# Kernel optimization log

Hardware: AMD Instinct MI355X
Metric: run time of the kernel (lower is better)

Reference implementation:

```python
import jax, jax.numpy as jnp
import numpy as np
from jax import lax

FEAT_STRIDE = 16
SCALES = (8, 16, 32)
RATIOS = (0.5, 1.0, 2.0)
PRE_NMS = 6000
POST_NMS = 300
NMS_THRESH = 0.7
MIN_SIZE = 16.0


def _base_anchors():
    base = 16.0
    cx = cy = base / 2.0
    anchors = []
    for r in RATIOS:
        for s in SCALES:
            h = base * s * np.sqrt(r)
            w = base * s * np.sqrt(1.0 / r)
            anchors.append([cx - w / 2, cy - h / 2, cx + w / 2, cy + h / 2])
    return np.asarray(anchors, np.float32)  # [A,4] (x1,y1,x2,y2)


def _shifted_anchors(h, w):
    base = _base_anchors()
    sy = np.arange(h, dtype=np.float32) * FEAT_STRIDE
    sx = np.arange(w, dtype=np.float32) * FEAT_STRIDE
    yy, xx = np.meshgrid(sy, sx, indexing='ij')  # h-major then w, matching NHWC permute
    shifts = np.stack([xx, yy, xx, yy], axis=-1).reshape(-1, 1, 4)
    return (shifts + base[None]).reshape(-1, 4).astype(np.float32)  # [h*w*A,4]


def _conv(x, w, b, pad):
    y = lax.conv_general_dilated(x, w, (1, 1), [(pad, pad), (pad, pad)],
                                 dimension_numbers=('NCHW', 'OIHW', 'NCHW'))
    return y + b[None, :, None, None]


def _iou(box, boxes):
    lt = jnp.maximum(box[:2], boxes[:, :2])
    rb = jnp.minimum(box[2:], boxes[:, 2:])
    wh = jnp.maximum(rb - lt, 0.0)
    inter = wh[:, 0] * wh[:, 1]
    a1 = (box[2] - box[0]) * (box[3] - box[1])
    a2 = (boxes[:, 2] - boxes[:, 0]) * (boxes[:, 3] - boxes[:, 1])
    return inter / (a1 + a2 - inter + 1e-9)


def _nms_proposals(boxes, scores):
    # boxes [K,4], scores [K] -> [POST_NMS,4]
    ws = boxes[:, 2] - boxes[:, 0]
    hs = boxes[:, 3] - boxes[:, 1]
    scores = jnp.where((ws >= MIN_SIZE) & (hs >= MIN_SIZE), scores, -jnp.inf)
    top_s, idx = lax.top_k(scores, PRE_NMS)
    b = boxes[idx]

    def body(i, st):
        keep, s = st
        j = jnp.argmax(s).astype(jnp.int32)
        keep = keep.at[i].set(j)
        sup = _iou(b[j], b) >= NMS_THRESH  # suppresses j itself too (iou=1)
        s = jnp.where(sup, -jnp.inf, s)
        return keep, s

    keep, _ = lax.fori_loop(0, POST_NMS, body,
                            (jnp.zeros((POST_NMS,), jnp.int32), top_s))
    return b[keep]


def setup_inputs() -> dict:
    key = jax.random.key(0)
    ks = jax.random.split(key, 5)
    n, c, h, w = 8, 512, 50, 64
    A = len(SCALES) * len(RATIOS)
    x = jax.random.normal(ks[0], (n, c, h, w), jnp.float32)
    w1 = jax.random.normal(ks[1], (512, 512, 3, 3), jnp.float32) * 0.02
    b1 = jnp.zeros((512,), jnp.float32)
    w_cls = jax.random.normal(ks[2], (A * 2, 512, 1, 1), jnp.float32) * 0.02
    b_cls = jnp.zeros((A * 2,), jnp.float32)
    w_bbox = jax.random.normal(ks[3], (A * 4, 512, 1, 1), jnp.float32) * 0.005
    b_bbox = jnp.zeros((A * 4,), jnp.float32)
    return {'x': x, 'w1': w1, 'b1': b1, 'w_cls': w_cls, 'b_cls': b_cls,
            'w_bbox': w_bbox, 'b_bbox': b_bbox}


def reference(x, w1, b1, w_cls, b_cls, w_bbox, b_bbox):
    n, _, h, w = x.shape
    A = len(SCALES) * len(RATIOS)
    img_h, img_w = h * FEAT_STRIDE, w * FEAT_STRIDE
    anchors = jnp.asarray(_shifted_anchors(h, w))  # [h*w*A,4]

    feat = jax.nn.relu(_conv(x, w1, b1, 1))
    cls = _conv(feat, w_cls, b_cls, 0).transpose(0, 2, 3, 1).reshape(n, h, w, A, 2)
    fg = jax.nn.softmax(cls, axis=-1)[..., 1].reshape(n, -1)  # [n, h*w*A]
    deltas = _conv(feat, w_bbox, b_bbox, 0).transpose(0, 2, 3, 1).reshape(n, -1, 4)

    # decode deltas against anchors
    aw = anchors[:, 2] - anchors[:, 0]
    ah = anchors[:, 3] - anchors[:, 1]
    acx = anchors[:, 0] + 0.5 * aw
    acy = anchors[:, 1] + 0.5 * ah
    cx = deltas[..., 0] * aw + acx
    cy = deltas[..., 1] * ah + acy
    pw = jnp.exp(deltas[..., 2]) * aw
    ph = jnp.exp(deltas[..., 3]) * ah
    boxes = jnp.stack([cx - 0.5 * pw, cy - 0.5 * ph,
                       cx + 0.5 * pw, cy + 0.5 * ph], axis=-1)  # [n,K,4]
    hi = jnp.asarray([img_w, img_h, img_w, img_h], jnp.float32)
    boxes = jnp.clip(boxes, 0.0, hi)

    rois = jax.vmap(_nms_proposals)(boxes, fg)  # [n,POST_NMS,4]
    roi_indices = jnp.repeat(jnp.arange(n, dtype=jnp.int32), POST_NMS)
    return rois.reshape(-1, 4), roi_indices
```

## Files before the change

### kernel.cpp

```cpp
#include <hip/hip_runtime.h>
#include <math.h>

#define NIMG 8
#define CIN  512
#define HF   50
#define WF   64
#define HW   3200
#define NA   9
#define KPER 28800
#define PRE  6000
#define POST 300

#define WHT_ELEMS  32768

#define NW    94
#define NCAP  6016

#define XTROWS 52
#define XTCOLS 66
#define XT_ELEMS ((size_t)NIMG * XTROWS * XTCOLS * CIN)
#define XT_BYTES (XT_ELEMS * 2)

#define WPK_ELEMS ((size_t)2 * 4 * 9 * 16 * 4096)
#define WPK_HALF  (4 * 9 * 16 * 4096)

#define SCALE_X 256.0f
#define SCALE_W 16384.0f
#define INV_SCALE (1.0f / 4194304.0f)

typedef _Float16 f16x8 __attribute__((ext_vector_type(8)));
typedef float f32x4  __attribute__((ext_vector_type(4)));
typedef unsigned short u16x8 __attribute__((ext_vector_type(8)));
typedef unsigned long long u64;

__constant__ float BASEA[9][4] = {
  {-82.509667991878083f, -37.254833995939042f,  98.509667991878083f,  53.254833995939042f},
  {-173.01933598375617f, -82.509667991878083f, 189.01933598375617f,   98.509667991878083f},
  {-354.03867196751233f, -173.01933598375617f, 370.03867196751233f,  189.01933598375617f},
  { -56.0f,  -56.0f,  72.0f,  72.0f},
  {-120.0f, -120.0f, 136.0f, 136.0f},
  {-248.0f, -248.0f, 264.0f, 264.0f},
  {-37.254833995939042f, -82.509667991878083f,  53.254833995939042f,  98.509667991878083f},
  {-82.509667991878083f, -173.01933598375617f,  98.509667991878083f, 189.01933598375617f},
  {-173.01933598375617f, -354.03867196751233f, 189.01933598375617f,  370.03867196751233f},
};

__device__ __forceinline__ unsigned int ordf(float f) {
  unsigned int u = __float_as_uint(f);
  return (u & 0x80000000u) ? ~u : (u | 0x80000000u);
}

__device__ __forceinline__ unsigned short f2h(float f) {
  union { _Float16 h; unsigned short u; } cv;
  cv.h = (_Float16)f;
  return cv.u;
}
__device__ __forceinline__ float h2f(unsigned short u) {
  union { _Float16 h; unsigned short u; } cv;
  cv.u = u;
  return (float)cv.h;
}

__global__ __launch_bounds__(256) void k_zerox(float4* __restrict__ a,
                                               float4* __restrict__ b) {
  const int tot = (int)(XT_BYTES / 16);
  const int stride = gridDim.x * 256;
  const float4 z = make_float4(0.f, 0.f, 0.f, 0.f);
  for (int i = blockIdx.x * 256 + threadIdx.x; i < tot; i += stride) {
    a[i] = z;
    b[i] = z;
  }
}

__global__ __launch_bounds__(256) void k_prepxT(const float4* __restrict__ x4,
                                                unsigned short* __restrict__ xh,
                                                unsigned short* __restrict__ xl) {
  __shared__ float tile[128][65];
  const int b = blockIdx.x;
  const int cic = b & 3;
  const int rest = b >> 2;
  const int hrow = rest % 50;
  const int n = rest / 50;
  const int t = threadIdx.x;
#pragma unroll
  for (int jj = 0; jj < 8; ++jj) {
    const int e = t + 256 * jj;
    const int row = e >> 4, c4 = e & 15;
    const float4 v = x4[(((size_t)(n * CIN + cic * 128 + row) * HF + hrow) << 4) + c4];
    tile[row][c4 * 4 + 0] = v.x;
    tile[row][c4 * 4 + 1] = v.y;
    tile[row][c4 * 4 + 2] = v.z;
    tile[row][c4 * 4 + 3] = v.w;
  }
  __syncthreads();
#pragma unroll
  for (int jj = 0; jj < 4; ++jj) {
    const int e = t + 256 * jj;
    const int w = e >> 4, c8 = e & 15;
    const size_t base = ((size_t)((n * XTROWS + (hrow + 1)) * XTCOLS) + (w + 1)) * CIN
                        + cic * 128 + c8 * 8;
    u16x8 hv, lv;
#pragma unroll
    for (int u = 0; u < 8; ++u) {
      const float g = tile[c8 * 8 + u][w] * SCALE_X;
      const unsigned short hh = f2h(g);
      hv[u] = (short)hh;
      lv[u] = (short)f2h(g - h2f(hh));
    }
    *reinterpret_cast<u16x8*>(xh + base) = hv;
    *reinterpret_cast<u16x8*>(xl + base) = lv;
  }
}

__global__ __launch_bounds__(256) void k_prepwPk(const float* __restrict__ w1,
                                                 unsigned short* __restrict__ wpk) {
  const int tot = (int)WPK_ELEMS;
  const int stride = gridDim.x * 256;
  for (int idx = blockIdx.x * 256 + threadIdx.x; idx < tot; idx += stride) {
    const int i = idx & 4095;
    int rest = idx >> 12;
    const int ks = rest & 15; rest >>= 4;
    const int tap = rest % 9; rest /= 9;
    const int cob = rest & 3;
    const int sp = rest >> 2;
    const int col = i >> 5;
    const int slotp = (i >> 3) & 3;
    const int j = i & 7;
    const int s = slotp ^ ((col >> 1) & 3);
    const int ci = ks * 32 + s * 8 + j;
    const int co = cob * 128 + col;
    const float g = w1[((size_t)co * CIN + ci) * 9 + tap] * SCALE_W;
    const unsigned short hh = f2h(g);
    wpk[idx] = sp ? f2h(g - h2f(hh)) : hh;
  }
}

__global__ __launch_bounds__(256) void k_preph(const float* __restrict__ wc,
                                               const float* __restrict__ bc,
                                               const float* __restrict__ wb,
                                               const float* __restrict__ bb,
                                               float* __restrict__ WHT2,
                                               float* __restrict__ bh) {
  const int TOT = WHT_ELEMS + 64;
  const int stride = gridDim.x * 256;
  for (int idx = blockIdx.x * 256 + threadIdx.x; idx < TOT; idx += stride) {
    if (idx < WHT_ELEMS) {
      int r = idx & 3;
      int o = (idx >> 2) & 63;
      int c = (idx >> 8) * 4 + r;
      float v = 0.0f;
      if (o < 18) v = wc[(size_t)o * CIN + c];
      else if (o < 54) v = wb[(size_t)(o - 18) * CIN + c];
      WHT2[idx] = v;
    } else {
      int o = idx - WHT_ELEMS;
      float v = 0.0f;
      if (o < 18) v = bc[o];
      else if (o < 54) v = bb[o - 18];
      bh[o] = v;
    }
  }
}

#define GLDS(gp, lp) __builtin_amdgcn_global_load_lds( \
    (const __attribute__((address_space(1))) unsigned int*)(gp), \
    (__attribute__((address_space(3))) unsigned int*)(lp), 16, 0, 0)

__global__ __launch_bounds__(256, 2) void k_convmfma(
    const unsigned short* __restrict__ xh,
    const unsigned short* __restrict__ xl,
    const unsigned short* __restrict__ wpk,
    const float* __restrict__ b1,
    float* __restrict__ feat) {
  __shared__ unsigned short lds[2][4][4096];

  const int pb  = blockIdx.x;
  const int cob = blockIdx.y;
  const int n   = pb / 25;
  const int h0  = (pb - n * 25) * 2;
  const int t   = threadIdx.x;
  const int wid = t >> 6;
  const int l   = t & 63;
  const int wm  = wid >> 1;
  const int wn  = wid & 1;

  const int colp = l >> 2;
  const int sB = (((l & 3) ^ ((l >> 3) & 3)) << 3);
  const unsigned short* xsrc = (wid == 3) ? xl : xh;
  const size_t wA_base = (size_t)(wid & 1) * WPK_HALF;

  const int fr = l & 15;
  const int fq = l >> 4;
  const int slotr = ((fq ^ ((fr >> 1) & 3)) << 4);

  f32x4 acc[4][4] = {};

  auto stage = [&](int sbuf, int ti) {
    const int ks  = ti / 9;
    const int tap = ti - ks * 9;
    if (wid < 2) {
      const unsigned short* gp = wpk + wA_base
          + ((size_t)((cob * 9 + tap) * 16 + ks) << 12) + l * 8;
      unsigned short* lp = &lds[sbuf][wid][0];
#pragma unroll
      for (int q = 0; q < 8; ++q)
        GLDS(gp + q * 512, lp + q * 512);
    } else {
      const int ky = (tap * 11) >> 5;
      const int kx = tap - ky * 3;
      const size_t ebase = ((size_t)((n * XTROWS + h0 + ky) * XTCOLS + kx + colp) << 9)
                           + ks * 32 + sB;
      unsigned short* lp = &lds[sbuf][wid][0];
#pragma unroll
      for (int q = 0; q < 8; ++q)
        GLDS(xsrc + ebase + ((size_t)(((q >> 2) * XTCOLS + (q & 3) * 16)) << 9),
             lp + q * 512);
    }
  };

  stage(0, 0);
  __syncthreads();

  int buf = 0;
  for (int ti = 0; ti < 144; ++ti) {
    if (ti < 143) stage(buf ^ 1, ti + 1);

    f16x8 ah[4], al[4], bhf[4], blf[4];
#pragma unroll
    for (int mi = 0; mi < 4; ++mi) {
      const int off = (((wm << 6) + (mi << 4) + fr) << 6) + slotr;
      ah[mi] = *(const f16x8*)((const char*)&lds[buf][0][0] + off);
      al[mi] = *(const f16x8*)((const char*)&lds[buf][1][0] + off);
    }
#pragma unroll
    for (int ni = 0; ni < 4; ++ni) {
      const int off = (((wn << 6) + (ni << 4) + fr) << 6) + slotr;
      bhf[ni] = *(const f16x8*)((const char*)&lds[buf][2][0] + off);
      blf[ni] = *(const f16x8*)((const char*)&lds[buf][3][0] + off);
    }
#pragma unroll
    for (int mi = 0; mi < 4; ++mi)
#pragma unroll
      for (int ni = 0; ni < 4; ++ni) {
        acc[mi][ni] = __builtin_amdgcn_mfma_f32_16x16x32_f16(ah[mi], bhf[ni], acc[mi][ni], 0, 0, 0);
        acc[mi][ni] = __builtin_amdgcn_mfma_f32_16x16x32_f16(ah[mi], blf[ni], acc[mi][ni], 0, 0, 0);
        acc[mi][ni] = __builtin_amdgcn_mfma_f32_16x16x32_f16(al[mi], bhf[ni], acc[mi][ni], 0, 0, 0);
      }
    __syncthreads();
    buf ^= 1;
  }

  const int h = h0 + wn;
#pragma unroll
  for (int mi = 0; mi < 4; ++mi) {
    const int co = (cob << 7) + (wm << 6) + (mi << 4) + (fq << 2);
    const float4 bias = *(const float4*)&b1[co];
#pragma unroll
    for (int ni = 0; ni < 4; ++ni) {
      const int w = (ni << 4) + fr;
      float4 v;
      v.x = fmaxf(fmaf(acc[mi][ni][0], INV_SCALE, bias.x), 0.0f);
      v.y = fmaxf(fmaf(acc[mi][ni][1], INV_SCALE, bias.y), 0.0f);
      v.z = fmaxf(fmaf(acc[mi][ni][2], INV_SCALE, bias.z), 0.0f);
      v.w = fmaxf(fmaf(acc[mi][ni][3], INV_SCALE, bias.w), 0.0f);
      *(float4*)(feat + (((size_t)n * HW + h * WF + w) << 9) + co) = v;
    }
  }
}

__global__ __launch_bounds__(256) void k_head(const float* __restrict__ feat,
                                              const float* __restrict__ WHT2,
                                              const float* __restrict__ bh,
                                              float* __restrict__ scores,
                                              float4* __restrict__ boxes) {
  __shared__ float fsh[16][512];
  __shared__ float vsh[16][64];
  const int t = threadIdx.x;
  const int wvid = t >> 6;
  const int o = t & 63;
  const int pos0 = blockIdx.x * 16;

  for (int i = t; i < 16 * 512; i += 256)
    fsh[i >> 9][i & 511] = feat[((size_t)pos0 << 9) + i];
  __syncthreads();

  {
    const int p0 = wvid * 4;
    float a0 = 0.f, a1 = 0.f, a2 = 0.f, a3 = 0.f;
    const float4* wp = reinterpret_cast<const float4*>(WHT2);
    const float4* f0 = reinterpret_cast<const float4*>(&fsh[p0 + 0][0]);
    const float4* f1 = reinterpret_cast<const float4*>(&fsh[p0 + 1][0]);
    const float4* f2 = reinterpret_cast<const float4*>(&fsh[p0 + 2][0]);
    const float4* f3 = reinterpret_cast<const float4*>(&fsh[p0 + 3][0]);
#pragma unroll 4
    for (int c4 = 0; c4 < 128; ++c4) {
      float4 w4 = wp[c4 * 64 + o];
      float4 v;
      v = f0[c4];
      a0 = fmaf(w4.x, v.x, a0); a0 = fmaf(w4.y, v.y, a0);
      a0 = fmaf(w4.z, v.z, a0); a0 = fmaf(w4.w, v.w, a0);
      v = f1[c4];
      a1 = fmaf(w4.x, v.x, a1); a1 = fmaf(w4.y, v.y, a1);
      a1 = fmaf(w4.z, v.z, a1); a1 = fmaf(w4.w, v.w, a1);
      v = f2[c4];
      a2 = fmaf(w4.x, v.x, a2); a2 = fmaf(w4.y, v.y, a2);
      a2 = fmaf(w4.z, v.z, a2); a2 = fmaf(w4.w, v.w, a2);
      v = f3[c4];
      a3 = fmaf(w4.x, v.x, a3); a3 = fmaf(w4.y, v.y, a3);
      a3 = fmaf(w4.z, v.z, a3); a3 = fmaf(w4.w, v.w, a3);
    }
    float bv = bh[o];
    vsh[p0 + 0][o] = a0 + bv;
    vsh[p0 + 1][o] = a1 + bv;
    vsh[p0 + 2][o] = a2 + bv;
    vsh[p0 + 3][o] = a3 + bv;
  }
  __syncthreads();

  if (t < 144) {
    const int p2 = t / 9, a = t % 9;
    const int pos = pos0 + p2;
    const int n = pos / HW;
    const int r = pos - n * HW;
    const int ph = r >> 6;
    const int pw = r & 63;

    float l0 = vsh[p2][a * 2];
    float l1 = vsh[p2][a * 2 + 1];
    float m  = fmaxf(l0, l1);
    float e0 = (float)exp((double)__fsub_rn(l0, m));
    float e1 = (float)exp((double)__fsub_rn(l1, m));
    float fg = __fdiv_rn(e1, __fadd_rn(e0, e1));

    float d0 = vsh[p2][18 + a * 4 + 0];
    float d1 = vsh[p2][18 + a * 4 + 1];
    float d2 = vsh[p2][18 + a * 4 + 2];
    float d3 = vsh[p2][18 + a * 4 + 3];

    float sx = (float)(pw * 16);
    float sy = (float)(ph * 16);
    float ax1 = __fadd_rn(BASEA[a][0], sx);
    float ay1 = __fadd_rn(BASEA[a][1], sy);
    float ax2 = __fadd_rn(BASEA[a][2], sx);
    float ay2 = __fadd_rn(BASEA[a][3], sy);
    float aw = __fsub_rn(ax2, ax1);
    float ah = __fsub_rn(ay2, ay1);
    float acx = __fadd_rn(ax1, __fmul_rn(0.5f, aw));
    float acy = __fadd_rn(ay1, __fmul_rn(0.5f, ah));
    float cx = __fadd_rn(__fmul_rn(d0, aw), acx);
    float cy = __fadd_rn(__fmul_rn(d1, ah), acy);
    float pwd = __fmul_rn((float)exp((double)d2), aw);
    float phd = __fmul_rn((float)exp((double)d3), ah);
    float x1 = __fsub_rn(cx, __fmul_rn(0.5f, pwd));
    float y1 = __fsub_rn(cy, __fmul_rn(0.5f, phd));
    float x2 = __fadd_rn(cx, __fmul_rn(0.5f, pwd));
    float y2 = __fadd_rn(cy, __fmul_rn(0.5f, phd));
    x1 = fminf(fmaxf(x1, 0.0f), 1024.0f);
    x2 = fminf(fmaxf(x2, 0.0f), 1024.0f);
    y1 = fminf(fmaxf(y1, 0.0f), 800.0f);
    y2 = fminf(fmaxf(y2, 0.0f), 800.0f);
    float wsz = __fsub_rn(x2, x1);
    float hsz = __fsub_rn(y2, y1);
    float sc = (wsz >= 16.0f && hsz >= 16.0f) ? fg : -__builtin_huge_valf();

    const int idx = n * KPER + r * NA + a;
    scores[idx] = sc;
    boxes[idx] = make_float4(x1, y1, x2, y2);
  }
}

__global__ __launch_bounds__(1024) void k_topk(const float* __restrict__ scores,
                                               u64* __restrict__ ckey) {
  const int n = blockIdx.x;
  const int t = threadIdx.x;
  __shared__ unsigned int hist[256];
  __shared__ unsigned int sh_selB, sh_ngt, sh_binc, sh_num;
  const float* sc = scores + (size_t)n * KPER;

  unsigned int prefix = 0, prefMask = 0, ngt = 0, neq = 0;
  for (int shift = 24; shift >= 0; shift -= 8) {
    if (t < 256) hist[t] = 0;
    __syncthreads();
    for (int i = t; i < KPER; i += 1024) {
      unsigned int u = ordf(sc[i]);
      if ((u & prefMask) == prefix) atomicAdd(&hist[(u >> shift) & 255], 1u);
    }
    __syncthreads();
    if (t == 0) {
      unsigned int cnt = ngt;
      for (int b = 255; b >= 0; --b) {
        unsigned int c = hist[b];
        if (cnt + c >= (unsigned)PRE) { sh_selB = (unsigned)b; sh_ngt = cnt; sh_binc = c; break; }
        cnt += c;
      }
    }
    __syncthreads();
    prefix |= (sh_selB << shift);
    prefMask |= (0xFFu << shift);
    ngt = sh_ngt;
    neq = sh_binc;
    __syncthreads();
  }
  const unsigned int T = prefix;
  const unsigned int needed = (unsigned)PRE - ngt;
  unsigned int J = 0xFFFFFFFFu;
  if (needed < neq) {
    if (t < 256) hist[t] = 0;
    __syncthreads();
    for (int i = t; i < KPER; i += 1024)
      if (ordf(sc[i]) == T) atomicAdd(&hist[i >> 7], 1u);
    __syncthreads();
    if (t == 0) {
      unsigned int cnt = 0;
      for (int b = 0; b < 256; ++b) {
        unsigned int c = hist[b];
        if (cnt + c >= needed) { sh_selB = (unsigned)b; sh_ngt = needed - cnt; break; }
        cnt += c;
      }
    }
    __syncthreads();
    const unsigned int selH = sh_selB;
    const unsigned int needLow = sh_ngt;
    __syncthreads();
    if (t < 128) hist[t] = 0;
    __syncthreads();
    for (int i = t; i < KPER; i += 1024)
      if (ordf(sc[i]) == T && ((unsigned)(i >> 7)) == selH) atomicAdd(&hist[i & 127], 1u);
    __syncthreads();
    if (t == 0) {
      unsigned int cnt = 0;
      for (int b = 0; b < 128; ++b) {
        unsigned int c = hist[b];
        if (cnt + c >= needLow) { sh_selB = (selH << 7) | (unsigned)b; break; }
        cnt += c;
      }
    }
    __syncthreads();
    J = sh_selB;
  }

  if (t == 0) sh_num = 0;
  __syncthreads();
  for (int i = t; i < KPER; i += 1024) {
    unsigned int u = ordf(sc[i]);
    bool in = (u > T) || (u == T && (unsigned)i <= J);
    if (in) {
      unsigned int p = atomicAdd(&sh_num, 1u);
      ckey[(size_t)n * PRE + p] = (((u64)u) << 32) | (u64)(~(unsigned int)i);
    }
  }
}

__global__ __launch_bounds__(1024) void k_sortc(const u64* __restrict__ ckey,
                                                const float4* __restrict__ boxes,
                                                float4* __restrict__ sbox,
                                                u64* __restrict__ valid) {
  __shared__ u64 sk[8192];
  const int n = blockIdx.x;
  const int t = threadIdx.x;
  for (int e = t; e < 8192; e += 1024)
    sk[e] = (e < PRE) ? ckey[(size_t)n * PRE + e] : 0ull;
  __syncthreads();
  for (int k = 2; k <= 8192; k <<= 1) {
    for (int j = k >> 1; j > 0; j >>= 1) {
      for (int p = t; p < 4096; p += 1024) {
        const int i = ((p & ~(j - 1)) << 1) | (p & (j - 1));
        const int ip = i | j;
        u64 a = sk[i], b = sk[ip];
        const bool desc = ((i & k) == 0);
        if ((a < b) == desc) { sk[i] = b; sk[ip] = a; }
      }
      __syncthreads();
    }
  }
  for (int e = t; e < NCAP; e += 1024) {
    float4 bx = make_float4(0.f, 0.f, 0.f, 0.f);
    if (e < PRE) {
      unsigned idx = ~(unsigned)(sk[e] & 0xFFFFFFFFull);
      bx = boxes[(size_t)n * KPER + idx];
    }
    sbox[(size_t)n * NCAP + e] = bx;
  }
  if (t < 128) {
    u64 w = 0;
    if (t < NW) {
      for (int b = 0; b < 64; ++b) {
        int e = t * 64 + b;
        if (e < PRE && ((sk[e] >> 32) > 0x007FFFFFull)) w |= 1ull << b;
      }
    }
    valid[n * 128 + t] = w;
  }
}

__global__ __launch_bounds__(64) void k_mask(const float4* __restrict__ sbox,
                                             u64* __restrict__ mask) {
  const int ib = blockIdx.x;
  const int jb = blockIdx.y;
  const int n  = blockIdx.z;
  const int r  = threadIdx.x;
  const int i  = ib * 64 + r;
  u64* mout = mask + ((size_t)(n * NCAP) + i) * NW + jb;
  if (jb < ib) { *mout = 0ull; return; }
  __shared__ float4 jbox[64];
  jbox[r] = sbox[(size_t)n * NCAP + jb * 64 + r];
  __syncthreads();
  const float4 p = sbox[(size_t)n * NCAP + i];
  const float pa = __fmul_rn(__fsub_rn(p.z, p.x), __fsub_rn(p.w, p.y));
  u64 word = 0;
#pragma unroll 8
  for (int b = 0; b < 64; ++b) {
    const float4 q = jbox[b];
    float ltx = fmaxf(p.x, q.x);
    float lty = fmaxf(p.y, q.y);
    float rbx = fminf(p.z, q.z);
    float rby = fminf(p.w, q.w);
    float wv = fmaxf(__fsub_rn(rbx, ltx), 0.0f);
    float hv = fmaxf(__fsub_rn(rby, lty), 0.0f);
    float inter = __fmul_rn(wv, hv);
    float a2 = __fmul_rn(__fsub_rn(q.z, q.x), __fsub_rn(q.w, q.y));
    float denom = __fadd_rn(__fsub_rn(__fadd_rn(pa, a2), inter), 1e-9f);
    float iou = __fdiv_rn(inter, denom);
    if (iou >= 0.7f) word |= (1ull << b);
  }
  *mout = word;
}

__global__ __launch_bounds__(64) void k_scan(const u64* __restrict__ mask,
                                             const u64* __restrict__ valid,
                                             const float4* __restrict__ sbox,
                                             float* __restrict__ out) {
  const int n = blockIdx.x;
  const int lane = threadIdx.x;
  u64 s0 = 0, s1 = 0;
  const u64 v0 = valid[n * 128 + 2 * lane];
  const u64 v1 = valid[n * 128 + 2 * lane + 1];
  const u64* mrow = mask + (size_t)n * NCAP * NW;
  __shared__ int keep_list[POST];
  int kept = 0;

  ulonglong2 cur[8], nxt[8];
#pragma unroll
  for (int r = 0; r < 8; ++r)
    cur[r] = ((const ulonglong2*)(mrow + (size_t)r * NW))[lane];

  for (int g = 0; g < PRE / 8; ++g) {
    if (kept >= POST) break;
    if (g < PRE / 8 - 1) {
#pragma unroll
      for (int r = 0; r < 8; ++r)
        nxt[r] = ((const ulonglong2*)(mrow + (size_t)((g + 1) * 8 + r) * NW))[lane];
    }
#pragma unroll
    for (int r = 0; r < 8; ++r) {
      if (kept < POST) {
        const int i = g * 8 + r;
        const int w = i >> 6;
        const u64 avail = (w & 1) ? (v1 & ~s1) : (v0 & ~s0);
        const unsigned h32 = (unsigned)(avail >> (i & 32));
        const unsigned wrd = __shfl(h32, w >> 1, 64);
        if ((wrd >> (i & 31)) & 1u) {
          if (lane == 0) keep_list[kept] = i;
          ++kept;
          s0 |= cur[r].x;
          s1 |= cur[r].y;
        }
      }
    }
#pragma unroll
    for (int r = 0; r < 8; ++r) cur[r] = nxt[r];
  }
  __syncthreads();

  for (int it = lane; it < POST; it += 64) {
    const int cand = (it < kept) ? keep_list[it] : 0;
    const float4 b = sbox[(size_t)n * NCAP + cand];
    float* orow = out + ((size_t)n * POST + it) * 4;
    orow[0] = b.x; orow[1] = b.y; orow[2] = b.z; orow[3] = b.w;
    out[(size_t)NIMG * POST * 4 + (size_t)n * POST + it] = (float)n;
  }
}

extern "C" void kernel_launch(void* const* d_in, const int* in_sizes, int n_in,
                              void* d_out, int out_size, void* d_ws, size_t ws_size,
                              hipStream_t stream) {
  const float* x    = (const float*)d_in[0];
  const float* w1   = (const float*)d_in[1];
  const float* b1   = (const float*)d_in[2];
  const float* wcls = (const float*)d_in[3];
  const float* bcls = (const float*)d_in[4];
  const float* wbb  = (const float*)d_in[5];
  const float* bbb  = (const float*)d_in[6];
  float* out = (float*)d_out;

  char* ws = (char*)d_ws;
  size_t off = 0;
  float* feat = (float*)(ws + off);               off += (size_t)NIMG * HW * CIN * 4;
  float* scores = (float*)(ws + off);             off += (size_t)NIMG * KPER * 4;
  float4* boxes = (float4*)(ws + off);            off += (size_t)NIMG * KPER * 16;
  u64* ckey = (u64*)(ws + off);                   off += (size_t)NIMG * PRE * 8;
  float4* sbox = (float4*)(ws + off);             off += (size_t)NIMG * NCAP * 16;
  u64* valid = (u64*)(ws + off);                  off += (size_t)NIMG * 128 * 8;
  u64* mask = (u64*)(ws + off);                   off += (size_t)NIMG * NCAP * NW * 8;
  float* WHT2 = (float*)(ws + off);               off += (size_t)WHT_ELEMS * 4;
  float* bh   = (float*)(ws + off);               off += 256;
  unsigned short* xTh = (unsigned short*)(ws + off); off += XT_BYTES;
  unsigned short* xTl = (unsigned short*)(ws + off); off += XT_BYTES;
  unsigned short* wpk = (unsigned short*)(ws + off); off += WPK_ELEMS * 2;

  k_zerox<<<2048, 256, 0, stream>>>((float4*)xTh, (float4*)xTl);
  k_prepxT<<<1600, 256, 0, stream>>>((const float4*)x, xTh, xTl);
  k_prepwPk<<<2048, 256, 0, stream>>>(w1, wpk);
  k_preph<<<128, 256, 0, stream>>>(wcls, bcls, wbb, bbb, WHT2, bh);
  k_convmfma<<<dim3(200, 4, 1), 256, 0, stream>>>(xTh, xTl, wpk, b1, feat);
  k_head<<<(NIMG * HW) / 16, 256, 0, stream>>>(feat, WHT2, bh, scores, boxes);
  k_topk<<<NIMG, 1024, 0, stream>>>(scores, ckey);
  k_sortc<<<NIMG, 1024, 0, stream>>>(ckey, boxes, sbox, valid);
  k_mask<<<dim3(NW, NW, NIMG), 64, 0, stream>>>(sbox, mask);
  k_scan<<<NIMG, 64, 0, stream>>>(mask, valid, sbox, out);
}
```

Before: 784.0 us.

## Fuse prep kernels, zero only halo, remap conv blocks, merge topk/sort, triangular mask

Merges the four preparation kernels into one launch and zeroes only the padding halo of the transposed input instead of the whole buffer. Conv blocks are remapped from a 1D grid so that each XCD works on one output-channel block and a contiguous range of pixel blocks, aiming at better L2 reuse. Top-k selection and the bitonic sort are merged so candidate keys stay in LDS instead of going through global memory. The IoU-mask kernel now launches only upper-triangular tile pairs, and the NMS scan prefetches 16 mask rows per step instead of 8. Lower-triangle mask words are no longer written, which assumes the scan never reads them.

```diff
diff --git a/kernel.cpp b/kernel.cpp
--- a/kernel.cpp
+++ b/kernel.cpp
@@ -15,6 +15,7 @@
 
 #define NW    94
 #define NCAP  6016
+#define NTRI  4465
 
 #define XTROWS 52
 #define XTCOLS 66
@@ -27,6 +28,15 @@
 #define SCALE_X 256.0f
 #define SCALE_W 16384.0f
 #define INV_SCALE (1.0f / 4194304.0f)
+
+#define PB_XT   1600
+#define PB_HALO 64
+#define PB_WPK  288
+#define PB_PH   16
+#define PB_TOT  (PB_XT + PB_HALO + PB_WPK + PB_PH)
+
+#define HALO_VPI 14848
+#define HALO_TOT (NIMG * HALO_VPI)
 
 typedef _Float16 f16x8 __attribute__((ext_vector_type(8)));
 typedef float f32x4  __attribute__((ext_vector_type(4)));
@@ -61,103 +71,113 @@
   return (float)cv.h;
 }
 
-__global__ __launch_bounds__(256) void k_zerox(float4* __restrict__ a,
-                                               float4* __restrict__ b) {
-  const int tot = (int)(XT_BYTES / 16);
-  const int stride = gridDim.x * 256;
-  const float4 z = make_float4(0.f, 0.f, 0.f, 0.f);
-  for (int i = blockIdx.x * 256 + threadIdx.x; i < tot; i += stride) {
-    a[i] = z;
-    b[i] = z;
-  }
-}
-
-__global__ __launch_bounds__(256) void k_prepxT(const float4* __restrict__ x4,
-                                                unsigned short* __restrict__ xh,
-                                                unsigned short* __restrict__ xl) {
+__global__ __launch_bounds__(256) void k_prep_all(
+    const float4* __restrict__ x4,
+    const float* __restrict__ w1,
+    const float* __restrict__ wc, const float* __restrict__ bc,
+    const float* __restrict__ wb, const float* __restrict__ bb,
+    unsigned short* __restrict__ xh, unsigned short* __restrict__ xl,
+    unsigned short* __restrict__ wpk,
+    float* __restrict__ WHT2, float* __restrict__ bh) {
   __shared__ float tile[128][65];
-  const int b = blockIdx.x;
-  const int cic = b & 3;
-  const int rest = b >> 2;
-  const int hrow = rest % 50;
-  const int n = rest / 50;
+  const int blk = blockIdx.x;
   const int t = threadIdx.x;
-#pragma unroll
-  for (int jj = 0; jj < 8; ++jj) {
-    const int e = t + 256 * jj;
-    const int row = e >> 4, c4 = e & 15;
-    const float4 v = x4[(((size_t)(n * CIN + cic * 128 + row) * HF + hrow) << 4) + c4];
-    tile[row][c4 * 4 + 0] = v.x;
-    tile[row][c4 * 4 + 1] = v.y;
-    tile[row][c4 * 4 + 2] = v.z;
-    tile[row][c4 * 4 + 3] = v.w;
-  }
-  __syncthreads();
-#pragma unroll
-  for (int jj = 0; jj < 4; ++jj) {
-    const int e = t + 256 * jj;
-    const int w = e >> 4, c8 = e & 15;
-    const size_t base = ((size_t)((n * XTROWS + (hrow + 1)) * XTCOLS) + (w + 1)) * CIN
-                        + cic * 128 + c8 * 8;
-    u16x8 hv, lv;
-#pragma unroll
-    for (int u = 0; u < 8; ++u) {
-      const float g = tile[c8 * 8 + u][w] * SCALE_X;
+
+  if (blk < PB_XT) {
+    const int cic = blk & 3;
+    const int rest = blk >> 2;
+    const int hrow = rest % 50;
+    const int n = rest / 50;
+#pragma unroll
+    for (int jj = 0; jj < 8; ++jj) {
+      const int e = t + 256 * jj;
+      const int row = e >> 4, c4 = e & 15;
+      const float4 v = x4[(((size_t)(n * CIN + cic * 128 + row) * HF + hrow) << 4) + c4];
+      tile[row][c4 * 4 + 0] = v.x;
+      tile[row][c4 * 4 + 1] = v.y;
+      tile[row][c4 * 4 + 2] = v.z;
+      tile[row][c4 * 4 + 3] = v.w;
+    }
+    __syncthreads();
+#pragma unroll
+    for (int jj = 0; jj < 4; ++jj) {
+      const int e = t + 256 * jj;
+      const int w = e >> 4, c8 = e & 15;
+      const size_t base = ((size_t)((n * XTROWS + (hrow + 1)) * XTCOLS) + (w + 1)) * CIN
+                          + cic * 128 + c8 * 8;
+      u16x8 hv, lv;
+#pragma unroll
+      for (int u = 0; u < 8; ++u) {
+        const float g = tile[c8 * 8 + u][w] * SCALE_X;
+        const unsigned short hh = f2h(g);
+        hv[u] = (short)hh;
+        lv[u] = (short)f2h(g - h2f(hh));
+      }
+      *reinterpret_cast<u16x8*>(xh + base) = hv;
+      *reinterpret_cast<u16x8*>(xl + base) = lv;
+    }
+  } else if (blk < PB_XT + PB_HALO) {
+    const u16x8 z = {0, 0, 0, 0, 0, 0, 0, 0};
+    const int tid = (blk - PB_XT) * 256 + t;
+    for (int v = tid; v < HALO_TOT; v += PB_HALO * 256) {
+      const int n = v / HALO_VPI;
+      const int r = v - n * HALO_VPI;
+      int row, col, v8;
+      if (r < 8448) {
+        row = (r < 4224) ? 0 : 51;
+        const int r2 = (r < 4224) ? r : r - 4224;
+        col = r2 >> 6;
+        v8 = r2 & 63;
+      } else {
+        const int q = r - 8448;
+        row = 1 + (q >> 7);
+        const int rr = q & 127;
+        col = (rr >= 64) ? 65 : 0;
+        v8 = rr & 63;
+      }
+      const size_t off = ((size_t)((n * XTROWS + row) * XTCOLS) + col) * CIN + v8 * 8;
+      *reinterpret_cast<u16x8*>(xh + off) = z;
+      *reinterpret_cast<u16x8*>(xl + off) = z;
+    }
+  } else if (blk < PB_XT + PB_HALO + PB_WPK) {
+    const int tot = (int)WPK_ELEMS;
+    const int tid = (blk - PB_XT - PB_HALO) * 256 + t;
+    for (int idx = tid; idx < tot; idx += PB_WPK * 256) {
+      const int i = idx & 4095;
+      int rest = idx >> 12;
+      const int ks = rest & 15; rest >>= 4;
+      const int tap = rest % 9; rest /= 9;
+      const int cob = rest & 3;
+      const int sp = rest >> 2;
+      const int col = i >> 5;
+      const int slotp = (i >> 3) & 3;
+      const int j = i & 7;
+      const int s = slotp ^ ((col >> 1) & 3);
+      const int ci = ks * 32 + s * 8 + j;
+      const int co = cob * 128 + col;
+      const float g = w1[((size_t)co * CIN + ci) * 9 + tap] * SCALE_W;
       const unsigned short hh = f2h(g);
-      hv[u] = (short)hh;
-      lv[u] = (short)f2h(g - h2f(hh));
-    }
-    *reinterpret_cast<u16x8*>(xh + base) = hv;
-    *reinterpret_cast<u16x8*>(xl + base) = lv;
-  }
-}
-
-__global__ __launch_bounds__(256) void k_prepwPk(const float* __restrict__ w1,
-                                                 unsigned short* __restrict__ wpk) {
-  const int tot = (int)WPK_ELEMS;
-  const int stride = gridDim.x * 256;
-  for (int idx = blockIdx.x * 256 + threadIdx.x; idx < tot; idx += stride) {
-    const int i = idx & 4095;
-    int rest = idx >> 12;
-    const int ks = rest & 15; rest >>= 4;
-    const int tap = rest % 9; rest /= 9;
-    const int cob = rest & 3;
-    const int sp = rest >> 2;
-    const int col = i >> 5;
-    const int slotp = (i >> 3) & 3;
-    const int j = i & 7;
-    const int s = slotp ^ ((col >> 1) & 3);
-    const int ci = ks * 32 + s * 8 + j;
-    const int co = cob * 128 + col;
-    const float g = w1[((size_t)co * CIN + ci) * 9 + tap] * SCALE_W;
-    const unsigned short hh = f2h(g);
-    wpk[idx] = sp ? f2h(g - h2f(hh)) : hh;
-  }
-}
-
-__global__ __launch_bounds__(256) void k_preph(const float* __restrict__ wc,
-                                               const float* __restrict__ bc,
-                                               const float* __restrict__ wb,
-                                               const float* __restrict__ bb,
-                                               float* __restrict__ WHT2,
-                                               float* __restrict__ bh) {
-  const int TOT = WHT_ELEMS + 64;
-  const int stride = gridDim.x * 256;
-  for (int idx = blockIdx.x * 256 + threadIdx.x; idx < TOT; idx += stride) {
-    if (idx < WHT_ELEMS) {
-      int r = idx & 3;
-      int o = (idx >> 2) & 63;
-      int c = (idx >> 8) * 4 + r;
-      float v = 0.0f;
-      if (o < 18) v = wc[(size_t)o * CIN + c];
-      else if (o < 54) v = wb[(size_t)(o - 18) * CIN + c];
-      WHT2[idx] = v;
-    } else {
-      int o = idx - WHT_ELEMS;
-      float v = 0.0f;
-      if (o < 18) v = bc[o];
-      else if (o < 54) v = bb[o - 18];
-      bh[o] = v;
+      wpk[idx] = sp ? f2h(g - h2f(hh)) : hh;
+    }
+  } else {
+    const int TOT = WHT_ELEMS + 64;
+    const int tid = (blk - PB_XT - PB_HALO - PB_WPK) * 256 + t;
+    for (int idx = tid; idx < TOT; idx += PB_PH * 256) {
+      if (idx < WHT_ELEMS) {
+        int r = idx & 3;
+        int o = (idx >> 2) & 63;
+        int c = (idx >> 8) * 4 + r;
+        float v = 0.0f;
+        if (o < 18) v = wc[(size_t)o * CIN + c];
+        else if (o < 54) v = wb[(size_t)(o - 18) * CIN + c];
+        WHT2[idx] = v;
+      } else {
+        int o = idx - WHT_ELEMS;
+        float v = 0.0f;
+        if (o < 18) v = bc[o];
+        else if (o < 54) v = bb[o - 18];
+        bh[o] = v;
+      }
     }
   }
 }
@@ -174,8 +194,12 @@
     float* __restrict__ feat) {
   __shared__ unsigned short lds[2][4][4096];
 
-  const int pb  = blockIdx.x;
-  const int cob = blockIdx.y;
+  const int raw = blockIdx.x;
+  const int xcd = raw & 7;
+  const int idx = raw >> 3;
+  const int cob = xcd >> 1;
+  const int pb  = (xcd & 1) * 100 + idx;
+
   const int n   = pb / 25;
   const int h0  = (pb - n * 25) * 2;
   const int t   = threadIdx.x;
@@ -369,13 +393,18 @@
   }
 }
 
-__global__ __launch_bounds__(1024) void k_topk(const float* __restrict__ scores,
-                                               u64* __restrict__ ckey) {
+__global__ __launch_bounds__(1024) void k_select(const float* __restrict__ scores,
+                                                 const float4* __restrict__ boxes,
+                                                 float4* __restrict__ sbox,
+                                                 u64* __restrict__ valid) {
+  __shared__ u64 sk[8192];
+  __shared__ unsigned int hist[256];
+  __shared__ unsigned int sh_selB, sh_ngt, sh_binc, sh_num;
   const int n = blockIdx.x;
   const int t = threadIdx.x;
-  __shared__ unsigned int hist[256];
-  __shared__ unsigned int sh_selB, sh_ngt, sh_binc, sh_num;
   const float* sc = scores + (size_t)n * KPER;
+
+  for (int e = t; e < 8192; e += 1024) sk[e] = 0ull;
 
   unsigned int prefix = 0, prefMask = 0, ngt = 0, neq = 0;
   for (int shift = 24; shift >= 0; shift -= 8) {
@@ -446,21 +475,11 @@
     bool in = (u > T) || (u == T && (unsigned)i <= J);
     if (in) {
       unsigned int p = atomicAdd(&sh_num, 1u);
-      ckey[(size_t)n * PRE + p] = (((u64)u) << 32) | (u64)(~(unsigned int)i);
-    }
-  }
-}
-
-__global__ __launch_bounds__(1024) void k_sortc(const u64* __restrict__ ckey,
-                                                const float4* __restrict__ boxes,
-                                                float4* __restrict__ sbox,
-                                                u64* __restrict__ valid) {
-  __shared__ u64 sk[8192];
-  const int n = blockIdx.x;
-  const int t = threadIdx.x;
-  for (int e = t; e < 8192; e += 1024)
-    sk[e] = (e < PRE) ? ckey[(size_t)n * PRE + e] : 0ull;
+      sk[p] = (((u64)u) << 32) | (u64)(~(unsigned int)i);
+    }
+  }
   __syncthreads();
+
   for (int k = 2; k <= 8192; k <<= 1) {
     for (int j = k >> 1; j > 0; j >>= 1) {
       for (int p = t; p < 4096; p += 1024) {
@@ -473,6 +492,7 @@
       __syncthreads();
     }
   }
+
   for (int e = t; e < NCAP; e += 1024) {
     float4 bx = make_float4(0.f, 0.f, 0.f, 0.f);
     if (e < PRE) {
@@ -495,26 +515,28 @@
 
 __global__ __launch_bounds__(64) void k_mask(const float4* __restrict__ sbox,
                                              u64* __restrict__ mask) {
-  const int ib = blockIdx.x;
-  const int jb = blockIdx.y;
-  const int n  = blockIdx.z;
-  const int r  = threadIdx.x;
-  const int i  = ib * 64 + r;
-  u64* mout = mask + ((size_t)(n * NCAP) + i) * NW + jb;
-  if (jb < ib) { *mout = 0ull; return; }
+  const int p = blockIdx.x;
+  const int n = blockIdx.y;
+  int ib = (int)((189.0 - sqrt(35721.0 - 8.0 * (double)p)) * 0.5);
+  while (94 * (ib + 1) - (ib * (ib + 1)) / 2 <= p) ++ib;
+  while (94 * ib - ((ib - 1) * ib) / 2 > p) --ib;
+  const int jb = ib + (p - (94 * ib - ((ib - 1) * ib) / 2));
+
+  const int r = threadIdx.x;
+  const int i = ib * 64 + r;
   __shared__ float4 jbox[64];
   jbox[r] = sbox[(size_t)n * NCAP + jb * 64 + r];
   __syncthreads();
-  const float4 p = sbox[(size_t)n * NCAP + i];
-  const float pa = __fmul_rn(__fsub_rn(p.z, p.x), __fsub_rn(p.w, p.y));
+  const float4 pbx = sbox[(size_t)n * NCAP + i];
+  const float pa = __fmul_rn(__fsub_rn(pbx.z, pbx.x), __fsub_rn(pbx.w, pbx.y));
   u64 word = 0;
 #pragma unroll 8
   for (int b = 0; b < 64; ++b) {
     const float4 q = jbox[b];
-    float ltx = fmaxf(p.x, q.x);
-    float lty = fmaxf(p.y, q.y);
-    float rbx = fminf(p.z, q.z);
-    float rby = fminf(p.w, q.w);
+    float ltx = fmaxf(pbx.x, q.x);
+    float lty = fmaxf(pbx.y, q.y);
+    float rbx = fminf(pbx.z, q.z);
+    float rby = fminf(pbx.w, q.w);
     float wv = fmaxf(__fsub_rn(rbx, ltx), 0.0f);
     float hv = fmaxf(__fsub_rn(rby, lty), 0.0f);
     float inter = __fmul_rn(wv, hv);
@@ -523,7 +545,7 @@
     float iou = __fdiv_rn(inter, denom);
     if (iou >= 0.7f) word |= (1ull << b);
   }
-  *mout = word;
+  mask[((size_t)(n * NCAP) + i) * NW + jb] = word;
 }
 
 __global__ __launch_bounds__(64) void k_scan(const u64* __restrict__ mask,
@@ -539,22 +561,22 @@
   __shared__ int keep_list[POST];
   int kept = 0;
 
-  ulonglong2 cur[8], nxt[8];
-#pragma unroll
-  for (int r = 0; r < 8; ++r)
+  ulonglong2 cur[16], nxt[16];
+#pragma unroll
+  for (int r = 0; r < 16; ++r)
     cur[r] = ((const ulonglong2*)(mrow + (size_t)r * NW))[lane];
 
-  for (int g = 0; g < PRE / 8; ++g) {
+  for (int g = 0; g < PRE / 16; ++g) {
     if (kept >= POST) break;
-    if (g < PRE / 8 - 1) {
-#pragma unroll
-      for (int r = 0; r < 8; ++r)
-        nxt[r] = ((const ulonglong2*)(mrow + (size_t)((g + 1) * 8 + r) * NW))[lane];
-    }
-#pragma unroll
-    for (int r = 0; r < 8; ++r) {
+    if (g < PRE / 16 - 1) {
+#pragma unroll
+      for (int r = 0; r < 16; ++r)
+        nxt[r] = ((const ulonglong2*)(mrow + (size_t)((g + 1) * 16 + r) * NW))[lane];
+    }
+#pragma unroll
+    for (int r = 0; r < 16; ++r) {
       if (kept < POST) {
-        const int i = g * 8 + r;
+        const int i = g * 16 + r;
         const int w = i >> 6;
         const u64 avail = (w & 1) ? (v1 & ~s1) : (v0 & ~s0);
         const unsigned h32 = (unsigned)(avail >> (i & 32));
@@ -568,7 +590,7 @@
       }
     }
 #pragma unroll
-    for (int r = 0; r < 8; ++r) cur[r] = nxt[r];
+    for (int r = 0; r < 16; ++r) cur[r] = nxt[r];
   }
   __syncthreads();
 
@@ -598,7 +620,6 @@
   float* feat = (float*)(ws + off);               off += (size_t)NIMG * HW * CIN * 4;
   float* scores = (float*)(ws + off);             off += (size_t)NIMG * KPER * 4;
   float4* boxes = (float4*)(ws + off);            off += (size_t)NIMG * KPER * 16;
-  u64* ckey = (u64*)(ws + off);                   off += (size_t)NIMG * PRE * 8;
   float4* sbox = (float4*)(ws + off);             off += (size_t)NIMG * NCAP * 16;
   u64* valid = (u64*)(ws + off);                  off += (size_t)NIMG * 128 * 8;
   u64* mask = (u64*)(ws + off);                   off += (size_t)NIMG * NCAP * NW * 8;
@@ -608,14 +629,11 @@
   unsigned short* xTl = (unsigned short*)(ws + off); off += XT_BYTES;
   unsigned short* wpk = (unsigned short*)(ws + off); off += WPK_ELEMS * 2;
 
-  k_zerox<<<2048, 256, 0, stream>>>((float4*)xTh, (float4*)xTl);
-  k_prepxT<<<1600, 256, 0, stream>>>((const float4*)x, xTh, xTl);
-  k_prepwPk<<<2048, 256, 0, stream>>>(w1, wpk);
-  k_preph<<<128, 256, 0, stream>>>(wcls, bcls, wbb, bbb, WHT2, bh);
-  k_convmfma<<<dim3(200, 4, 1), 256, 0, stream>>>(xTh, xTl, wpk, b1, feat);
+  k_prep_all<<<PB_TOT, 256, 0, stream>>>((const float4*)x, w1, wcls, bcls, wbb, bbb,
+                                         xTh, xTl, wpk, WHT2, bh);
+  k_convmfma<<<800, 256, 0, stream>>>(xTh, xTl, wpk, b1, feat);
   k_head<<<(NIMG * HW) / 16, 256, 0, stream>>>(feat, WHT2, bh, scores, boxes);
-  k_topk<<<NIMG, 1024, 0, stream>>>(scores, ckey);
-  k_sortc<<<NIMG, 1024, 0, stream>>>(ckey, boxes, sbox, valid);
-  k_mask<<<dim3(NW, NW, NIMG), 64, 0, stream>>>(sbox, mask);
+  k_select<<<NIMG, 1024, 0, stream>>>(scores, boxes, sbox, valid);
+  k_mask<<<dim3(NTRI, NIMG), 64, 0, stream>>>(sbox, mask);
   k_scan<<<NIMG, 64, 0, stream>>>(mask, valid, sbox, out);
 }
```

Result: faster. 756.6 us (-3.5%).
